# Kernel tuning notes

Hardware: AMD Instinct MI355X
Metric: run time of the kernel (lower is better)

The kernel has to match this reference:

```python
import jax, jax.numpy as jnp
import numpy as np

K, STRIDE, PAD = 3, 1, 1


def _unfold(x, k=K, stride=STRIDE, pad=PAD):
    # x: [B, C, H, W] -> patches [B, C*k*k, L] (im2col, torch nn.Unfold layout:
    # channel index = c*k*k + ki*k + kj)
    p = jax.lax.conv_general_dilated_patches(
        x, filter_shape=(k, k), window_strides=(stride, stride),
        padding=((pad, pad), (pad, pad)))  # [B, C*k*k, Ho, Wo]
    B = x.shape[0]
    return p.reshape(B, p.shape[1], -1)


def reference(x, weight, dweight, bias):
    B, C, H, W = x.shape
    O = weight.shape[0]
    cols = _unfold(x)                                   # [B, C*k*k, L]
    # scalar gate per spatial position: dweight . sigmoid(cols)
    gate = jnp.einsum('f,bfl->bl', dweight.reshape(-1), jax.nn.sigmoid(cols))
    gated = cols * gate[:, None, :]                     # [B, C*k*k, L]
    out = jnp.einsum('of,bfl->bol', weight.reshape(O, -1), gated)  # [B, O, L]
    out = out + bias[None, :, None]
    Ho, Wo = (H // 2, W // 2) if STRIDE == 2 else (H, W)
    return out.reshape(B, O, Ho, Wo)


def setup_inputs() -> dict:
    key = jax.random.key(0)
    k1, k2, k3, k4 = jax.random.split(key, 4)
    B, C, O, H, W = 8, 32, 32, 256, 256
    fan_out = O * K * K
    std = float(np.sqrt(2.0 / fan_out))
    return {
        'x': jax.random.normal(k1, (B, C, H, W), dtype=jnp.float32),
        'weight': jax.random.normal(k2, (O, C, K, K), dtype=jnp.float32) * std,
        'dweight': jax.random.normal(k3, (1, C, K, K), dtype=jnp.float32) * std,
        'bias': jax.random.normal(k4, (O,), dtype=jnp.float32),
    }
```

## Files before the change

kernel.cpp:

```cpp
#include <hip/hip_runtime.h>


typedef _Float16 half8 __attribute__((ext_vector_type(8)));
typedef _Float16 half2 __attribute__((ext_vector_type(2)));
typedef float f32x16 __attribute__((ext_vector_type(16)));

#define BATCH 8
#define CIN 32
#define COUT 32
#define TW 32
#define TH 8
#define HTW 34
#define HTH 10
#define CSTR 40
#define NCHUNK 18
#define NLDSA 14
#define NREGA (NCHUNK - NLDSA)
#define NPOS (HTH*HTW)

__global__ __launch_bounds__(256) void prep_pack(const float* __restrict__ w,
                                                 const float* __restrict__ dw,
                                                 _Float16* __restrict__ Apack,
                                                 half2* __restrict__ dwf2) {
  int t = blockIdx.x * 256 + threadIdx.x;
  if (t < 9216) {
    int q = t >> 9, lane = (t >> 3) & 63, j = t & 7;
    int tap = q >> 1, h = q & 1;
    int o = lane & 31, lh = lane >> 5;
    int c = h * 16 + lh * 8 + j;
    Apack[t] = (_Float16)w[o * 288 + c * 9 + tap];
  } else if (t < 9216 + 144) {
    int i = t - 9216;
    int cp = i / 9, tap = i - cp * 9;
    half2 d;
    d.x = (_Float16)dw[(2 * cp) * 9 + tap];
    d.y = (_Float16)dw[(2 * cp + 1) * 9 + tap];
    dwf2[i] = d;
  }
}

__global__ __launch_bounds__(512, 5) void dynconv(
    const float* __restrict__ x, const _Float16* __restrict__ Apack,
    const half2* __restrict__ dwf2, const float* __restrict__ bias,
    float* __restrict__ out) {
  __shared__ __align__(16) _Float16 lvA[NLDSA * 512];
  __shared__ __align__(16) _Float16 lv[NPOS * CSTR];
  __shared__ _Float16 gpart[9 * NPOS];

  const int bid0 = blockIdx.x;
  const int bb = bid0 & 7, idx = bid0 >> 3;
  const int xt = idx & 7, yt = idx >> 3;
  const int x0 = xt * TW, y0 = yt * TH;
  const int tid = threadIdx.x;
  const int lane = tid & 63;

  half8 acopy0 = *(const half8*)(Apack + (tid << 3));
  half8 acopy1;
  if (tid < NLDSA * 64 - 512)
    acopy1 = *(const half8*)(Apack + ((512 + tid) << 3));

  const bool owner = tid < NPOS;
  float v[CIN];
  if (owner) {
    const int yy = tid / HTW, xx = tid - (tid / HTW) * HTW;
    const int gy = y0 + yy - 1, gx = x0 + xx - 1;
    const int voff = (gy << 8) + gx;
    if ((unsigned)gy < 256u && (unsigned)gx < 256u) {
#pragma unroll
      for (int c = 0; c < CIN; ++c)
        v[c] = x[(((size_t)(bb * CIN + c)) << 16) + voff];
    } else {
#pragma unroll
      for (int c = 0; c < CIN; ++c) v[c] = 0.f;
    }
  }

  *(half8*)(lvA + (tid << 3)) = acopy0;
  if (tid < NLDSA * 64 - 512)
    *(half8*)(lvA + ((512 + tid) << 3)) = acopy1;

  asm volatile("s_waitcnt vmcnt(0)" ::: "memory");

  if (owner) {
    float p[9];
#pragma unroll
    for (int tap = 0; tap < 9; ++tap) p[tap] = 0.f;
    _Float16 hv[CIN];
#pragma unroll
    for (int cp = 0; cp < CIN / 2; ++cp) {
      const float v0 = v[2 * cp], v1 = v[2 * cp + 1];
      const float s0 = __builtin_amdgcn_rcpf(1.f + __expf(-v0));
      const float s1 = __builtin_amdgcn_rcpf(1.f + __expf(-v1));
      half2 s2;
      s2.x = (_Float16)s0;
      s2.y = (_Float16)s1;
      hv[2 * cp] = (_Float16)v0;
      hv[2 * cp + 1] = (_Float16)v1;
#pragma unroll
      for (int tap = 0; tap < 9; ++tap) {
        const half2 d2 = dwf2[cp * 9 + tap];
#if __has_builtin(__builtin_amdgcn_fdot2)
        p[tap] = __builtin_amdgcn_fdot2(s2, d2, p[tap], false);
#else
        p[tap] += (float)s2.x * (float)d2.x + (float)s2.y * (float)d2.y;
#endif
      }
    }
#pragma unroll
    for (int u = 0; u < 4; ++u)
      *(half8*)(lv + tid * CSTR + u * 8) = *(const half8*)(hv + u * 8);
#pragma unroll
    for (int tap = 0; tap < 9; ++tap)
      gpart[tap * NPOS + tid] = (_Float16)p[tap];
  }

  half8 areg[NREGA];
#pragma unroll
  for (int r = 0; r < NREGA; ++r)
    areg[r] = *(const half8*)(Apack + (((NLDSA + r) * 64 + lane) << 3));

  __syncthreads();

  const int w8 = tid >> 6;
  const int ln = lane & 31, lh = lane >> 5;

  float gate = 0.f;
#pragma unroll
  for (int ki = 0; ki < 3; ++ki)
#pragma unroll
    for (int kj = 0; kj < 3; ++kj)
      gate += (float)gpart[(ki * 3 + kj) * NPOS + (w8 + ki) * HTW + ln + kj];

  f32x16 acc;
#pragma unroll
  for (int i = 0; i < 16; ++i) acc[i] = 0.f;

#pragma unroll
  for (int q = 0; q < NCHUNK; ++q) {
    const int tap = q >> 1, h = q & 1;
    const int ki = tap / 3, kj = tap - ki * 3;
    const half8 a = (q < NLDSA)
                        ? *(const half8*)(lvA + ((q * 64 + lane) << 3))
                        : areg[q - NLDSA];
    const int off = ((w8 + ki) * HTW + ln + kj) * CSTR + h * 16 + lh * 8;
    const half8 bv = *(const half8*)(lv + off);
    acc = __builtin_amdgcn_mfma_f32_32x32x16_f16(a, bv, acc, 0, 0, 0);
  }

  const int voff_out = ((y0 + w8) << 8) + x0 + ln;
#pragma unroll
  for (int reg = 0; reg < 16; ++reg) {
    const int o = (reg & 3) + 8 * (reg >> 2) + 4 * lh;
    out[(((size_t)(bb * COUT + o)) << 16) + voff_out] = acc[reg] * gate + bias[o];
  }
}

extern "C" void kernel_launch(void* const* d_in, const int* in_sizes, int n_in,
                              void* d_out, int out_size, void* d_ws, size_t ws_size,
                              hipStream_t stream) {
  const float* x    = (const float*)d_in[0];
  const float* wgt  = (const float*)d_in[1];
  const float* dw   = (const float*)d_in[2];
  const float* bias = (const float*)d_in[3];
  float* out = (float*)d_out;

  _Float16* Apack = (_Float16*)d_ws;
  half2* dwf2     = (half2*)((char*)d_ws + 18432);

  prep_pack<<<(9216 + 144 + 255) / 256, 256, 0, stream>>>(wgt, dw, Apack, dwf2);
  dynconv<<<BATCH * 32 * 8, 512, 0, stream>>>(x, Apack, dwf2, bias, out);
}
```

Measured before the change: 129.1 us.

## Stage input halo tile into LDS via direct global-to-LDS loads

Replaces per-thread strided global loads of 32 channels per halo position with cooperative 16-byte global_load_lds transfers into an LDS staging arena. The arena is then reused for the fp16 B tile and gate partials. Threads read their channel values from LDS before computing the sigmoid gate. This aims to coalesce global reads and drop the per-thread scattered loads, at the cost of extra barriers, a larger LDS footprint, and lower occupancy (launch bounds reduced from 5 to 4).

```diff
diff --git a/kernel.cpp b/kernel.cpp
--- a/kernel.cpp
+++ b/kernel.cpp
@@ -12,6 +12,7 @@
 #define TH 8
 #define HTW 34
 #define HTH 10
+#define XW 40
 #define CSTR 40
 #define NCHUNK 18
 #define NLDSA 14
@@ -39,13 +40,16 @@
   }
 }
 
-__global__ __launch_bounds__(512, 5) void dynconv(
+__global__ __launch_bounds__(512, 4) void dynconv(
     const float* __restrict__ x, const _Float16* __restrict__ Apack,
     const half2* __restrict__ dwf2, const float* __restrict__ bias,
     float* __restrict__ out) {
+  __shared__ __align__(16) unsigned char arena[32 * HTH * XW * 4];
   __shared__ __align__(16) _Float16 lvA[NLDSA * 512];
-  __shared__ __align__(16) _Float16 lv[NPOS * CSTR];
-  __shared__ _Float16 gpart[9 * NPOS];
+
+  float* xstage = (float*)arena;
+  _Float16* lv = (_Float16*)arena;
+  _Float16* gpart = (_Float16*)(arena + NPOS * CSTR * 2);
 
   const int bid0 = blockIdx.x;
   const int bb = bid0 & 7, idx = bid0 >> 3;
@@ -53,39 +57,58 @@
   const int x0 = xt * TW, y0 = yt * TH;
   const int tid = threadIdx.x;
   const int lane = tid & 63;
+  const int w8 = tid >> 6;
 
   half8 acopy0 = *(const half8*)(Apack + (tid << 3));
   half8 acopy1;
   if (tid < NLDSA * 64 - 512)
     acopy1 = *(const half8*)(Apack + ((512 + tid) << 3));
+  *(half8*)(lvA + (tid << 3)) = acopy0;
+  if (tid < NLDSA * 64 - 512)
+    *(half8*)(lvA + ((512 + tid) << 3)) = acopy1;
+
+#pragma unroll
+  for (int k = 0; k < 4; ++k) {
+    const int c = (k << 3) | w8;
+#pragma unroll
+    for (int j = 0; j < 2; ++j) {
+      const int u = (j << 6) | lane;
+      if (u < HTH * (XW / 4)) {
+        const int r = u / (XW / 4);
+        const int g = u - r * (XW / 4);
+        int gy = y0 + r - 1;
+        gy = gy < 0 ? 0 : (gy > 255 ? 255 : gy);
+        int gc = x0 - 4 + (g << 2);
+        gc = gc < 0 ? 0 : (gc > 252 ? 252 : gc);
+        const float* src = x + (((size_t)(bb * CIN + c)) << 16) + (gy << 8) + gc;
+        __builtin_amdgcn_global_load_lds(
+            (const __attribute__((address_space(1))) void*)src,
+            (__attribute__((address_space(3))) void*)(xstage + c * (HTH * XW) + (j << 8)),
+            16, 0, 0);
+      }
+    }
+  }
+
+  __syncthreads();
 
   const bool owner = tid < NPOS;
-  float v[CIN];
+  float p[9];
+  _Float16 hv[CIN];
   if (owner) {
     const int yy = tid / HTW, xx = tid - (tid / HTW) * HTW;
     const int gy = y0 + yy - 1, gx = x0 + xx - 1;
-    const int voff = (gy << 8) + gx;
+    float v[CIN];
     if ((unsigned)gy < 256u && (unsigned)gx < 256u) {
+      const int base = yy * XW + xx + 3;
 #pragma unroll
       for (int c = 0; c < CIN; ++c)
-        v[c] = x[(((size_t)(bb * CIN + c)) << 16) + voff];
+        v[c] = xstage[c * (HTH * XW) + base];
     } else {
 #pragma unroll
       for (int c = 0; c < CIN; ++c) v[c] = 0.f;
     }
-  }
-
-  *(half8*)(lvA + (tid << 3)) = acopy0;
-  if (tid < NLDSA * 64 - 512)
-    *(half8*)(lvA + ((512 + tid) << 3)) = acopy1;
-
-  asm volatile("s_waitcnt vmcnt(0)" ::: "memory");
-
-  if (owner) {
-    float p[9];
 #pragma unroll
     for (int tap = 0; tap < 9; ++tap) p[tap] = 0.f;
-    _Float16 hv[CIN];
 #pragma unroll
     for (int cp = 0; cp < CIN / 2; ++cp) {
       const float v0 = v[2 * cp], v1 = v[2 * cp + 1];
@@ -106,6 +129,11 @@
 #endif
       }
     }
+  }
+
+  __syncthreads();
+
+  if (owner) {
 #pragma unroll
     for (int u = 0; u < 4; ++u)
       *(half8*)(lv + tid * CSTR + u * 8) = *(const half8*)(hv + u * 8);
@@ -121,7 +149,6 @@
 
   __syncthreads();
 
-  const int w8 = tid >> 6;
   const int ln = lane & 31, lh = lane >> 5;
 
   float gate = 0.f;
```

New measurement: 142.4 us. 10.4% more time.
